# Performance work log

Hardware: AMD Instinct MI355X
Metric: run time of the kernel (lower is better)

Reference implementation:

```python
import jax, jax.numpy as jnp
import numpy as np


def setup_inputs() -> dict:
    key = jax.random.key(0)
    k1, k2, k3, k4, k5 = jax.random.split(key, 5)
    N, C, A = 4096, 64, 256
    fc_weight = jax.random.normal(k1, (C, A), dtype=jnp.float32) * 0.05
    features = jax.random.normal(k2, (N, A), dtype=jnp.float32)
    pred = jax.random.normal(k3, (N, C), dtype=jnp.float32)
    labels = jax.random.randint(k4, (N,), 0, C, dtype=jnp.int64)
    # make covariance PSD-ish and small-scale like class-conditional feature covariances
    B = jax.random.normal(k5, (C, A, A), dtype=jnp.float32) * 0.05
    covariance_sample = jnp.einsum('cij,ckj->cik', B, B)  # [C, A, A]
    Lambda = jnp.float32(0.5)
    return {
        'fc_weight': fc_weight,
        'features': features,
        'pred': pred,
        'labels': labels,
        'Lambda': Lambda,
        'covariance_sample': covariance_sample,
    }


def reference(fc_weight, features, pred, labels, Lambda, covariance_sample):
    # fc_weight: [C, A]; pred: [N, C]; labels: [N]; covariance_sample: [C, A, A]
    # ISDA-style augmentation: sigma2[n, c] = (w_c - w_{y_n})^T CV[y_n] (w_c - w_{y_n})
    # torch code builds N×C×C bmm and extracts diagonal; here we compute the
    # quadratic-form diagonal directly (same math, no redundant C× compute).
    labels = labels.astype(jnp.int32)
    diff = fc_weight[None, :, :] - fc_weight[labels][:, None, :]   # [N, C, A]
    cv = covariance_sample[labels]                                  # [N, A, A]
    tmp = jnp.einsum('nca,nab->ncb', diff, cv)                      # [N, C, A]
    sigma2 = Lambda * jnp.einsum('ncb,ncb->nc', tmp, diff)          # [N, C]
    aug_y = pred + 0.5 * sigma2
    # mean cross-entropy (nn.CrossEntropyLoss default reduction='mean')
    logp = jax.nn.log_softmax(aug_y, axis=-1)
    nll = -jnp.take_along_axis(logp, labels[:, None], axis=1)[:, 0]
    return jnp.mean(nll)
```

## Files before the change

kernel.cpp:

```cpp
#include <hip/hip_runtime.h>

#define N_ROWS 4096
#define C_CLS  64
#define A_DIM  256
#define BK     32
#define KCHUNK (A_DIM / BK)
#define GRID   (C_CLS * KCHUNK)

__device__ float    g_Spart[KCHUNK * C_CLS * C_CLS];
__device__ float    g_part[GRID];
__device__ unsigned g_bar  = 0;
__device__ unsigned g_tick = 0;

__global__ __launch_bounds__(256, 2) void fused_kernel(
    const float* __restrict__ W,
    const float* __restrict__ CV,
    const float* __restrict__ pred,
    const int*   __restrict__ labels,
    const float* __restrict__ lambda_p,
    float* __restrict__ out)
{
    __shared__ float Vt[BK][A_DIM];
    __shared__ float Dt[BK][C_CLS];
    __shared__ float Psum[32][C_CLS];
    __shared__ float wsum4[4];
    __shared__ int   s_last;

    const int t = threadIdx.x;

    {
        const int y  = blockIdx.x >> 3;
        const int kc = blockIdx.x & 7;
        const int kb = kc * BK;

        {
            const float4* src = (const float4*)(CV + ((size_t)y * A_DIM * A_DIM
                                                      + (size_t)kb * A_DIM));
            float4* vdst = (float4*)&Vt[0][0];
            #pragma unroll
            for (int i = 0; i < (BK * A_DIM / 4) / 256; ++i)
                vdst[t + i * 256] = src[t + i * 256];
        }

        {
            const int kq    = (t & 7) * 4;
            const int chalf = t >> 3;
            const float4 wy = *(const float4*)(W + y * A_DIM + kb + kq);
            #pragma unroll
            for (int cc = 0; cc < 2; ++cc) {
                const int c = chalf + cc * 32;
                const float4 wc = *(const float4*)(W + c * A_DIM + kb + kq);
                Dt[kq + 0][c] = wc.x - wy.x;
                Dt[kq + 1][c] = wc.y - wy.y;
                Dt[kq + 2][c] = wc.z - wy.z;
                Dt[kq + 3][c] = wc.w - wy.w;
            }
        }
        __syncthreads();

        const int c0 = (t & 7) * 8;
        const int a0 = (t >> 3) * 8;
        float acc[8][8];
        #pragma unroll
        for (int i = 0; i < 8; ++i)
            #pragma unroll
            for (int j = 0; j < 8; ++j) acc[i][j] = 0.0f;

        #pragma unroll 2
        for (int k = 0; k < BK; ++k) {
            const float4 a_lo = *(const float4*)&Vt[k][a0];
            const float4 a_hi = *(const float4*)&Vt[k][a0 + 4];
            const float4 d_lo = *(const float4*)&Dt[k][c0];
            const float4 d_hi = *(const float4*)&Dt[k][c0 + 4];
            const float af[8] = {a_lo.x, a_lo.y, a_lo.z, a_lo.w,
                                 a_hi.x, a_hi.y, a_hi.z, a_hi.w};
            const float df[8] = {d_lo.x, d_lo.y, d_lo.z, d_lo.w,
                                 d_hi.x, d_hi.y, d_hi.z, d_hi.w};
            #pragma unroll
            for (int i = 0; i < 8; ++i)
                #pragma unroll
                for (int j = 0; j < 8; ++j)
                    acc[i][j] += df[i] * af[j];
        }

        float s[8];
        {
            const float4 wy_lo = *(const float4*)(W + y * A_DIM + a0);
            const float4 wy_hi = *(const float4*)(W + y * A_DIM + a0 + 4);
            const float wyv[8] = {wy_lo.x, wy_lo.y, wy_lo.z, wy_lo.w,
                                  wy_hi.x, wy_hi.y, wy_hi.z, wy_hi.w};
            #pragma unroll
            for (int i = 0; i < 8; ++i) {
                const int c = c0 + i;
                const float4 wc_lo = *(const float4*)(W + c * A_DIM + a0);
                const float4 wc_hi = *(const float4*)(W + c * A_DIM + a0 + 4);
                const float wcv[8] = {wc_lo.x, wc_lo.y, wc_lo.z, wc_lo.w,
                                      wc_hi.x, wc_hi.y, wc_hi.z, wc_hi.w};
                float ss = 0.0f;
                #pragma unroll
                for (int j = 0; j < 8; ++j)
                    ss += acc[i][j] * (wcv[j] - wyv[j]);
                s[i] = ss;
            }
        }
        const int ag = t >> 3;
        *(float4*)&Psum[ag][c0]     = make_float4(s[0], s[1], s[2], s[3]);
        *(float4*)&Psum[ag][c0 + 4] = make_float4(s[4], s[5], s[6], s[7]);
        __syncthreads();

        if (t < C_CLS) {
            float r = 0.0f;
            #pragma unroll
            for (int g = 0; g < 32; ++g) r += Psum[g][t];
            __hip_atomic_store(&g_Spart[kc * C_CLS * C_CLS + y * C_CLS + t], r,
                               __ATOMIC_RELAXED, __HIP_MEMORY_SCOPE_AGENT);
        }
    }

    __syncthreads();
    if (t == 0) {
        unsigned v = __hip_atomic_fetch_add(&g_bar, 1u, __ATOMIC_RELAXED,
                                            __HIP_MEMORY_SCOPE_AGENT) + 1u;
        const unsigned target = (v + (GRID - 1u)) & ~(unsigned)(GRID - 1u);
        while (__hip_atomic_load(&g_bar, __ATOMIC_RELAXED,
                                 __HIP_MEMORY_SCOPE_AGENT) < target)
            __builtin_amdgcn_s_sleep(64);
        asm volatile("" ::: "memory");
    }
    __syncthreads();

    {
        const int lane = t & 63;
        const int wv   = t >> 6;
        const int gw   = (int)blockIdx.x * 4 + wv;
        const float lam = 0.5f * lambda_p[0];

        float acc_nll = 0.0f;
        #pragma unroll
        for (int r = 0; r < 2; ++r) {
            const int n = r * 2048 + gw;
            const int y = labels[n];
            float sp = 0.0f;
            #pragma unroll
            for (int k = 0; k < KCHUNK; ++k)
                sp += __hip_atomic_load(&g_Spart[k * C_CLS * C_CLS + y * C_CLS + lane],
                                        __ATOMIC_RELAXED, __HIP_MEMORY_SCOPE_AGENT);
            const float logit = pred[n * C_CLS + lane] + lam * sp;

            float m = logit;
            #pragma unroll
            for (int off = 32; off > 0; off >>= 1)
                m = fmaxf(m, __shfl_xor(m, off, 64));
            float e = __expf(logit - m);
            float ssum = e;
            #pragma unroll
            for (int off = 32; off > 0; off >>= 1)
                ssum += __shfl_xor(ssum, off, 64);
            const float ly = __shfl(logit, y, 64);
            acc_nll += logf(ssum) + m - ly;
        }

        if (lane == 0) wsum4[wv] = acc_nll;
        __syncthreads();
        if (t == 0) {
            __hip_atomic_store(&g_part[blockIdx.x],
                               wsum4[0] + wsum4[1] + wsum4[2] + wsum4[3],
                               __ATOMIC_RELAXED, __HIP_MEMORY_SCOPE_AGENT);
            asm volatile("s_waitcnt vmcnt(0)" ::: "memory");
            unsigned v = __hip_atomic_fetch_add(&g_tick, 1u, __ATOMIC_RELAXED,
                                                __HIP_MEMORY_SCOPE_AGENT) + 1u;
            s_last = ((v & (GRID - 1u)) == 0u) ? 1 : 0;
        }
        __syncthreads();

        if (s_last) {
            float v = __hip_atomic_load(&g_part[t], __ATOMIC_RELAXED,
                                        __HIP_MEMORY_SCOPE_AGENT)
                    + __hip_atomic_load(&g_part[t + 256], __ATOMIC_RELAXED,
                                        __HIP_MEMORY_SCOPE_AGENT);
            #pragma unroll
            for (int off = 32; off > 0; off >>= 1)
                v += __shfl_xor(v, off, 64);
            if (lane == 0) wsum4[wv] = v;
            __syncthreads();
            if (t == 0)
                out[0] = (wsum4[0] + wsum4[1] + wsum4[2] + wsum4[3])
                         * (1.0f / (float)N_ROWS);
        }
    }
}

extern "C" void kernel_launch(void* const* d_in, const int* in_sizes, int n_in,
                              void* d_out, int out_size, void* d_ws, size_t ws_size,
                              hipStream_t stream) {
    (void)in_sizes; (void)n_in; (void)out_size; (void)d_ws; (void)ws_size;
    const float* W      = (const float*)d_in[0];
    const float* pred   = (const float*)d_in[2];
    const int*   labels = (const int*)d_in[3];
    const float* lam    = (const float*)d_in[4];
    const float* CV     = (const float*)d_in[5];
    float* out = (float*)d_out;

    fused_kernel<<<dim3(GRID), dim3(256), 0, stream>>>(W, CV, pred, labels, lam, out);
}
```

Baseline: 105.3 us.

## Split fused kernel into quadratic-form and loss kernels, dropping grid barrier

```diff
diff --git a/kernel.cpp b/kernel.cpp
--- a/kernel.cpp
+++ b/kernel.cpp
@@ -5,188 +5,180 @@
 #define A_DIM  256
 #define BK     32
 #define KCHUNK (A_DIM / BK)
-#define GRID   (C_CLS * KCHUNK)
+#define LOSS_BLOCKS 256
 
 __device__ float    g_Spart[KCHUNK * C_CLS * C_CLS];
-__device__ float    g_part[GRID];
-__device__ unsigned g_bar  = 0;
+__device__ float    g_part[LOSS_BLOCKS];
 __device__ unsigned g_tick = 0;
 
-__global__ __launch_bounds__(256, 2) void fused_kernel(
+__global__ __launch_bounds__(256) void qform_kernel(
     const float* __restrict__ W,
-    const float* __restrict__ CV,
+    const float* __restrict__ CV)
+{
+    __shared__ float Vt[BK][A_DIM];
+    __shared__ float Dt[BK][C_CLS];
+    __shared__ float Psum[32][C_CLS];
+
+    const int t  = threadIdx.x;
+    const int y  = blockIdx.x >> 3;
+    const int kc = blockIdx.x & 7;
+    const int kb = kc * BK;
+
+    {
+        const float4* src = (const float4*)(CV + ((size_t)y * A_DIM * A_DIM
+                                                  + (size_t)kb * A_DIM));
+        float4* vdst = (float4*)&Vt[0][0];
+        #pragma unroll
+        for (int i = 0; i < (BK * A_DIM / 4) / 256; ++i)
+            vdst[t + i * 256] = src[t + i * 256];
+    }
+
+    {
+        const int kq    = (t & 7) * 4;
+        const int chalf = t >> 3;
+        const float4 wy = *(const float4*)(W + y * A_DIM + kb + kq);
+        #pragma unroll
+        for (int cc = 0; cc < 2; ++cc) {
+            const int c = chalf + cc * 32;
+            const float4 wc = *(const float4*)(W + c * A_DIM + kb + kq);
+            Dt[kq + 0][c] = wc.x - wy.x;
+            Dt[kq + 1][c] = wc.y - wy.y;
+            Dt[kq + 2][c] = wc.z - wy.z;
+            Dt[kq + 3][c] = wc.w - wy.w;
+        }
+    }
+    __syncthreads();
+
+    const int c0 = (t & 7) * 8;
+    const int a0 = (t >> 3) * 8;
+    float acc[8][8];
+    #pragma unroll
+    for (int i = 0; i < 8; ++i)
+        #pragma unroll
+        for (int j = 0; j < 8; ++j) acc[i][j] = 0.0f;
+
+    #pragma unroll 2
+    for (int k = 0; k < BK; ++k) {
+        const float4 a_lo = *(const float4*)&Vt[k][a0];
+        const float4 a_hi = *(const float4*)&Vt[k][a0 + 4];
+        const float4 d_lo = *(const float4*)&Dt[k][c0];
+        const float4 d_hi = *(const float4*)&Dt[k][c0 + 4];
+        const float af[8] = {a_lo.x, a_lo.y, a_lo.z, a_lo.w,
+                             a_hi.x, a_hi.y, a_hi.z, a_hi.w};
+        const float df[8] = {d_lo.x, d_lo.y, d_lo.z, d_lo.w,
+                             d_hi.x, d_hi.y, d_hi.z, d_hi.w};
+        #pragma unroll
+        for (int i = 0; i < 8; ++i)
+            #pragma unroll
+            for (int j = 0; j < 8; ++j)
+                acc[i][j] += df[i] * af[j];
+    }
+
+    float s[8];
+    {
+        const float4 wy_lo = *(const float4*)(W + y * A_DIM + a0);
+        const float4 wy_hi = *(const float4*)(W + y * A_DIM + a0 + 4);
+        const float wyv[8] = {wy_lo.x, wy_lo.y, wy_lo.z, wy_lo.w,
+                              wy_hi.x, wy_hi.y, wy_hi.z, wy_hi.w};
+        #pragma unroll
+        for (int i = 0; i < 8; ++i) {
+            const int c = c0 + i;
+            const float4 wc_lo = *(const float4*)(W + c * A_DIM + a0);
+            const float4 wc_hi = *(const float4*)(W + c * A_DIM + a0 + 4);
+            const float wcv[8] = {wc_lo.x, wc_lo.y, wc_lo.z, wc_lo.w,
+                                  wc_hi.x, wc_hi.y, wc_hi.z, wc_hi.w};
+            float ss = 0.0f;
+            #pragma unroll
+            for (int j = 0; j < 8; ++j)
+                ss += acc[i][j] * (wcv[j] - wyv[j]);
+            s[i] = ss;
+        }
+    }
+    const int ag = t >> 3;
+    *(float4*)&Psum[ag][c0]     = make_float4(s[0], s[1], s[2], s[3]);
+    *(float4*)&Psum[ag][c0 + 4] = make_float4(s[4], s[5], s[6], s[7]);
+    __syncthreads();
+
+    if (t < C_CLS) {
+        float r = 0.0f;
+        #pragma unroll
+        for (int g = 0; g < 32; ++g) r += Psum[g][t];
+        g_Spart[kc * C_CLS * C_CLS + y * C_CLS + t] = r;
+    }
+}
+
+__global__ __launch_bounds__(256) void loss_kernel(
     const float* __restrict__ pred,
     const int*   __restrict__ labels,
     const float* __restrict__ lambda_p,
     float* __restrict__ out)
 {
-    __shared__ float Vt[BK][A_DIM];
-    __shared__ float Dt[BK][C_CLS];
-    __shared__ float Psum[32][C_CLS];
-    __shared__ float wsum4[4];
+    __shared__ float wsum[4];
     __shared__ int   s_last;
 
-    const int t = threadIdx.x;
+    const int t    = threadIdx.x;
+    const int lane = t & 63;
+    const int wv   = t >> 6;
+    const int gw   = (int)blockIdx.x * 4 + wv;
+    const float lam = 0.5f * lambda_p[0];
 
-    {
-        const int y  = blockIdx.x >> 3;
-        const int kc = blockIdx.x & 7;
-        const int kb = kc * BK;
-
-        {
-            const float4* src = (const float4*)(CV + ((size_t)y * A_DIM * A_DIM
-                                                      + (size_t)kb * A_DIM));
-            float4* vdst = (float4*)&Vt[0][0];
-            #pragma unroll
-            for (int i = 0; i < (BK * A_DIM / 4) / 256; ++i)
-                vdst[t + i * 256] = src[t + i * 256];
-        }
-
-        {
-            const int kq    = (t & 7) * 4;
-            const int chalf = t >> 3;
-            const float4 wy = *(const float4*)(W + y * A_DIM + kb + kq);
-            #pragma unroll
-            for (int cc = 0; cc < 2; ++cc) {
-                const int c = chalf + cc * 32;
-                const float4 wc = *(const float4*)(W + c * A_DIM + kb + kq);
-                Dt[kq + 0][c] = wc.x - wy.x;
-                Dt[kq + 1][c] = wc.y - wy.y;
-                Dt[kq + 2][c] = wc.z - wy.z;
-                Dt[kq + 3][c] = wc.w - wy.w;
-            }
-        }
-        __syncthreads();
-
-        const int c0 = (t & 7) * 8;
-        const int a0 = (t >> 3) * 8;
-        float acc[8][8];
+    int ys[4];
+    #pragma unroll
+    for (int r = 0; r < 4; ++r) ys[r] = labels[r * 1024 + gw];
+    float pv[4];
+    #pragma unroll
+    for (int r = 0; r < 4; ++r) pv[r] = pred[(size_t)(r * 1024 + gw) * C_CLS + lane];
+    float sp[4];
+    #pragma unroll
+    for (int r = 0; r < 4; ++r) {
+        float s = 0.0f;
         #pragma unroll
-        for (int i = 0; i < 8; ++i)
-            #pragma unroll
-            for (int j = 0; j < 8; ++j) acc[i][j] = 0.0f;
-
-        #pragma unroll 2
-        for (int k = 0; k < BK; ++k) {
-            const float4 a_lo = *(const float4*)&Vt[k][a0];
-            const float4 a_hi = *(const float4*)&Vt[k][a0 + 4];
-            const float4 d_lo = *(const float4*)&Dt[k][c0];
-            const float4 d_hi = *(const float4*)&Dt[k][c0 + 4];
-            const float af[8] = {a_lo.x, a_lo.y, a_lo.z, a_lo.w,
-                                 a_hi.x, a_hi.y, a_hi.z, a_hi.w};
-            const float df[8] = {d_lo.x, d_lo.y, d_lo.z, d_lo.w,
-                                 d_hi.x, d_hi.y, d_hi.z, d_hi.w};
-            #pragma unroll
-            for (int i = 0; i < 8; ++i)
-                #pragma unroll
-                for (int j = 0; j < 8; ++j)
-                    acc[i][j] += df[i] * af[j];
-        }
-
-        float s[8];
-        {
-            const float4 wy_lo = *(const float4*)(W + y * A_DIM + a0);
-            const float4 wy_hi = *(const float4*)(W + y * A_DIM + a0 + 4);
-            const float wyv[8] = {wy_lo.x, wy_lo.y, wy_lo.z, wy_lo.w,
-                                  wy_hi.x, wy_hi.y, wy_hi.z, wy_hi.w};
-            #pragma unroll
-            for (int i = 0; i < 8; ++i) {
-                const int c = c0 + i;
-                const float4 wc_lo = *(const float4*)(W + c * A_DIM + a0);
-                const float4 wc_hi = *(const float4*)(W + c * A_DIM + a0 + 4);
-                const float wcv[8] = {wc_lo.x, wc_lo.y, wc_lo.z, wc_lo.w,
-                                      wc_hi.x, wc_hi.y, wc_hi.z, wc_hi.w};
-                float ss = 0.0f;
-                #pragma unroll
-                for (int j = 0; j < 8; ++j)
-                    ss += acc[i][j] * (wcv[j] - wyv[j]);
-                s[i] = ss;
-            }
-        }
-        const int ag = t >> 3;
-        *(float4*)&Psum[ag][c0]     = make_float4(s[0], s[1], s[2], s[3]);
-        *(float4*)&Psum[ag][c0 + 4] = make_float4(s[4], s[5], s[6], s[7]);
-        __syncthreads();
-
-        if (t < C_CLS) {
-            float r = 0.0f;
-            #pragma unroll
-            for (int g = 0; g < 32; ++g) r += Psum[g][t];
-            __hip_atomic_store(&g_Spart[kc * C_CLS * C_CLS + y * C_CLS + t], r,
-                               __ATOMIC_RELAXED, __HIP_MEMORY_SCOPE_AGENT);
-        }
+        for (int k = 0; k < KCHUNK; ++k)
+            s += g_Spart[k * C_CLS * C_CLS + ys[r] * C_CLS + lane];
+        sp[r] = s;
     }
 
+    float acc_nll = 0.0f;
+    #pragma unroll
+    for (int r = 0; r < 4; ++r) {
+        const float logit = pv[r] + lam * sp[r];
+        float m = logit;
+        #pragma unroll
+        for (int off = 32; off > 0; off >>= 1)
+            m = fmaxf(m, __shfl_xor(m, off, 64));
+        float e = __expf(logit - m);
+        float ssum = e;
+        #pragma unroll
+        for (int off = 32; off > 0; off >>= 1)
+            ssum += __shfl_xor(ssum, off, 64);
+        const float ly = __shfl(logit, ys[r], 64);
+        acc_nll += logf(ssum) + m - ly;
+    }
+
+    if (lane == 0) wsum[wv] = acc_nll;
     __syncthreads();
     if (t == 0) {
-        unsigned v = __hip_atomic_fetch_add(&g_bar, 1u, __ATOMIC_RELAXED,
+        __hip_atomic_store(&g_part[blockIdx.x],
+                           wsum[0] + wsum[1] + wsum[2] + wsum[3],
+                           __ATOMIC_RELAXED, __HIP_MEMORY_SCOPE_AGENT);
+        asm volatile("s_waitcnt vmcnt(0)" ::: "memory");
+        unsigned v = __hip_atomic_fetch_add(&g_tick, 1u, __ATOMIC_RELAXED,
                                             __HIP_MEMORY_SCOPE_AGENT) + 1u;
-        const unsigned target = (v + (GRID - 1u)) & ~(unsigned)(GRID - 1u);
-        while (__hip_atomic_load(&g_bar, __ATOMIC_RELAXED,
-                                 __HIP_MEMORY_SCOPE_AGENT) < target)
-            __builtin_amdgcn_s_sleep(64);
-        asm volatile("" ::: "memory");
+        s_last = ((v & (LOSS_BLOCKS - 1u)) == 0u) ? 1 : 0;
     }
     __syncthreads();
 
-    {
-        const int lane = t & 63;
-        const int wv   = t >> 6;
-        const int gw   = (int)blockIdx.x * 4 + wv;
-        const float lam = 0.5f * lambda_p[0];
-
-        float acc_nll = 0.0f;
+    if (s_last) {
+        float v = __hip_atomic_load(&g_part[t], __ATOMIC_RELAXED,
+                                    __HIP_MEMORY_SCOPE_AGENT);
         #pragma unroll
-        for (int r = 0; r < 2; ++r) {
-            const int n = r * 2048 + gw;
-            const int y = labels[n];
-            float sp = 0.0f;
-            #pragma unroll
-            for (int k = 0; k < KCHUNK; ++k)
-                sp += __hip_atomic_load(&g_Spart[k * C_CLS * C_CLS + y * C_CLS + lane],
-                                        __ATOMIC_RELAXED, __HIP_MEMORY_SCOPE_AGENT);
-            const float logit = pred[n * C_CLS + lane] + lam * sp;
-
-            float m = logit;
-            #pragma unroll
-            for (int off = 32; off > 0; off >>= 1)
-                m = fmaxf(m, __shfl_xor(m, off, 64));
-            float e = __expf(logit - m);
-            float ssum = e;
-            #pragma unroll
-            for (int off = 32; off > 0; off >>= 1)
-                ssum += __shfl_xor(ssum, off, 64);
-            const float ly = __shfl(logit, y, 64);
-            acc_nll += logf(ssum) + m - ly;
-        }
-
-        if (lane == 0) wsum4[wv] = acc_nll;
+        for (int off = 32; off > 0; off >>= 1)
+            v += __shfl_xor(v, off, 64);
+        if (lane == 0) wsum[wv] = v;
         __syncthreads();
-        if (t == 0) {
-            __hip_atomic_store(&g_part[blockIdx.x],
-                               wsum4[0] + wsum4[1] + wsum4[2] + wsum4[3],
-                               __ATOMIC_RELAXED, __HIP_MEMORY_SCOPE_AGENT);
-            asm volatile("s_waitcnt vmcnt(0)" ::: "memory");
-            unsigned v = __hip_atomic_fetch_add(&g_tick, 1u, __ATOMIC_RELAXED,
-                                                __HIP_MEMORY_SCOPE_AGENT) + 1u;
-            s_last = ((v & (GRID - 1u)) == 0u) ? 1 : 0;
-        }
-        __syncthreads();
-
-        if (s_last) {
-            float v = __hip_atomic_load(&g_part[t], __ATOMIC_RELAXED,
-                                        __HIP_MEMORY_SCOPE_AGENT)
-                    + __hip_atomic_load(&g_part[t + 256], __ATOMIC_RELAXED,
-                                        __HIP_MEMORY_SCOPE_AGENT);
-            #pragma unroll
-            for (int off = 32; off > 0; off >>= 1)
-                v += __shfl_xor(v, off, 64);
-            if (lane == 0) wsum4[wv] = v;
-            __syncthreads();
-            if (t == 0)
-                out[0] = (wsum4[0] + wsum4[1] + wsum4[2] + wsum4[3])
-                         * (1.0f / (float)N_ROWS);
-        }
+        if (t == 0)
+            out[0] = (wsum[0] + wsum[1] + wsum[2] + wsum[3])
+                     * (1.0f / (float)N_ROWS);
     }
 }
 
@@ -201,5 +193,6 @@
     const float* CV     = (const float*)d_in[5];
     float* out = (float*)d_out;
 
-    fused_kernel<<<dim3(GRID), dim3(256), 0, stream>>>(W, CV, pred, labels, lam, out);
+    qform_kernel<<<dim3(C_CLS * KCHUNK), dim3(256), 0, stream>>>(W, CV);
+    loss_kernel<<<dim3(LOSS_BLOCKS), dim3(256), 0, stream>>>(pred, labels, lam, out);
 }
```

Result: faster. 91.40 us (-13.2%).
